# Kernel tuning notes

Measured on AMD Instinct MI355X. Metric: run time of the kernel, lower is better.

## Reference

```python
import jax, jax.numpy as jnp
import numpy as np


def _conv1x1(x, w, b=None):
    # x: [B, Cin, N, S], w: [Cout, Cin], 1x1 Conv2d
    y = jnp.einsum('oc,bcns->bons', w, x)
    if b is not None:
        y = y + b[None, :, None, None]
    return y


def setup_inputs() -> dict:
    key = jax.random.key(0)
    ks = jax.random.split(key, 16)
    B, Cin, N, K = 4, 128, 16384, 16
    MID, OUT, SHARE, PT = 64, 128, 8, 10
    s = 0.05
    inp = {
        'sm_feats': jax.random.normal(ks[0], (B, Cin, N, K), jnp.float32),
        'sm_ppfs': jax.random.normal(ks[1], (B, PT, N, K), jnp.float32),
        'conv0_w': jax.random.normal(ks[2], (OUT, Cin), jnp.float32) * s,
        'conv0_b': jax.random.normal(ks[3], (OUT,), jnp.float32) * s,
        'conv1_w': jax.random.normal(ks[4], (MID, OUT), jnp.float32) * s,
        'conv1_b': jax.random.normal(ks[5], (MID,), jnp.float32) * s,
        'conv2_w': jax.random.normal(ks[6], (MID, OUT), jnp.float32) * s,
        'conv2_b': jax.random.normal(ks[7], (MID,), jnp.float32) * s,
        'conv3_w': jax.random.normal(ks[8], (MID, OUT), jnp.float32) * s,
        'conv3_b': jax.random.normal(ks[9], (MID,), jnp.float32) * s,
        'convw1_w': jax.random.normal(ks[10], (MID // SHARE, MID * K), jnp.float32) * s,
        'convw2_w': jax.random.normal(ks[11], (K * MID // SHARE, MID // SHARE), jnp.float32) * s,
        'convw2_b': jax.random.normal(ks[12], (K * MID // SHARE,), jnp.float32) * s,
        'convout_w': jax.random.normal(ks[13], (OUT, MID), jnp.float32) * s,
        'convout_b': jax.random.normal(ks[14], (OUT,), jnp.float32) * s,
        'pt1_w': jax.random.normal(ks[15], (MID, PT), jnp.float32) * s,
        'pt2_w': jax.random.normal(jax.random.fold_in(key, 99), (MID, MID), jnp.float32) * s,
    }
    return inp


def reference(sm_feats, sm_ppfs, conv0_w, conv0_b, conv1_w, conv1_b, conv2_w, conv2_b,
              conv3_w, conv3_b, convw1_w, convw2_w, convw2_b, convout_w, convout_b,
              pt1_w, pt2_w):
    xn = jax.nn.relu(_conv1x1(sm_feats, conv0_w, conv0_b))  # [B, OUT, N, K]
    x = xn[..., :1]                                          # center point feature
    identity = x
    x1 = _conv1x1(x, conv1_w, conv1_b)       # [B, MID, N, 1]
    x2 = _conv1x1(xn, conv2_w, conv2_b)      # [B, MID, N, K]
    x3 = _conv1x1(xn, conv3_w, conv3_b)      # [B, MID, N, K]
    ptf = _conv1x1(jax.nn.relu(_conv1x1(sm_ppfs, pt1_w)), pt2_w)  # [B, MID, N, K]
    x3 = x3 + ptf
    xfs = x1 - x2 + ptf                      # [B, MID, N, K]
    B, MID, N, K = xfs.shape
    share = MID // convw1_w.shape[0]
    xfs = jnp.transpose(xfs, (0, 1, 3, 2)).reshape(B, MID * K, 1, N)
    h = jax.nn.relu(_conv1x1(xfs, convw1_w))            # [B, MID//share, 1, N]
    w = _conv1x1(h, convw2_w, convw2_b)                  # [B, K*MID//share, 1, N]
    w = jax.nn.softmax(w.reshape(B, MID // share, K, N), axis=2)
    w = jnp.transpose(w, (0, 1, 3, 2))                   # [B, MID//share, N, K]
    w = jnp.tile(w, (1, share, 1, 1))                    # [B, MID, N, K]
    out = jax.nn.relu(jnp.sum(w * x3, axis=3, keepdims=True))  # [B, MID, N, 1]
    out = (_conv1x1(out, convout_w, convout_b) + identity).squeeze(3)  # [B, OUT, N]
    return out
```

## Files before the change

kernel.cpp:

```cpp
#include <hip/hip_runtime.h>
#include <hip/hip_bf16.h>


typedef __attribute__((ext_vector_type(8))) short bf16x8;
typedef __attribute__((ext_vector_type(4))) float f32x4;
typedef __attribute__((ext_vector_type(4))) unsigned short us4;

#define MFMA(a, b, c) __builtin_amdgcn_mfma_f32_16x16x32_bf16((a), (b), (c), 0, 0, 0)

#define OFF_F    0
#define OFF_X2   0
#define OFF_PTF  17408
#define OFF_XN   34816
#define OFF_X3   34816
#define OFF_XFS  52224
#define OFF_P    69632
#define OFF_WS   69632
#define OFF_HB   74752
#define OFF_OM   76288
#define OFF_X1   77824
#define OFF_XC   78912
#define SMEM_BYTES 81088

#define WS_W0  0
#define WS_W1  16384
#define WS_W2  24576
#define WS_W3  32768
#define WS_P1  40960
#define WS_P2  43008
#define WS_CW1 47104
#define WS_WO  63488
#define WS_TOTAL 71680

__device__ __forceinline__ unsigned short f2b(float f) {
    union { __hip_bfloat16 h; unsigned short u; } v;
    v.h = __float2bfloat16(f);
    return v.u;
}
__device__ __forceinline__ float b2f(unsigned short u) {
    union { unsigned u; float f; } v;
    v.u = ((unsigned)u) << 16;
    return v.f;
}
__device__ __forceinline__ us4 pk4(float a, float b, float c, float d) {
    us4 r; r[0] = f2b(a); r[1] = f2b(b); r[2] = f2b(c); r[3] = f2b(d); return r;
}
__device__ __forceinline__ bf16x8 ldb(const unsigned short* p) {
    return *(const bf16x8*)p;
}

__global__ __launch_bounds__(512, 1)
void convert_weights(const float* __restrict__ w0, const float* __restrict__ w1,
                     const float* __restrict__ w2, const float* __restrict__ w3,
                     const float* __restrict__ p1, const float* __restrict__ p2,
                     const float* __restrict__ cw1, const float* __restrict__ wo,
                     unsigned short* __restrict__ ws) {
    int i = blockIdx.x * 512 + threadIdx.x;
    if (i >= WS_TOTAL) return;
    float v;
    if (i < 16384)      v = w0[i];
    else if (i < 24576) v = w1[i - 16384];
    else if (i < 32768) v = w2[i - 24576];
    else if (i < 40960) v = w3[i - 32768];
    else if (i < 43008) { int r = i - 40960, row = r >> 5, k = r & 31;
                          v = (k < 10) ? p1[row * 10 + k] : 0.f; }
    else if (i < 47104) v = p2[i - 43008];
    else if (i < 63488) { int r = i - 47104, j = r >> 10, kc = r & 1023;
                          v = (j < 8) ? cw1[j * 1024 + (kc & 63) * 16 + (kc >> 6)] : 0.f; }
    else                v = wo[i - 63488];
    ws[i] = f2b(v);
}

__global__ __launch_bounds__(512, 4)
void fused_model_kernel(const float* __restrict__ feats, const float* __restrict__ ppfs,
                        const unsigned short* __restrict__ wsb,
                        const float* __restrict__ b0, const float* __restrict__ b1,
                        const float* __restrict__ b2, const float* __restrict__ b3,
                        const float* __restrict__ cw2, const float* __restrict__ cb2,
                        const float* __restrict__ bo, float* __restrict__ out) {
    extern __shared__ char smem[];
    const int tid = threadIdx.x;
    const int W = tid >> 6;
    const int lane = tid & 63;
    const int kk = lane & 15;
    const int g = lane >> 4;
    const int bid = blockIdx.x;
    const int b = bid >> 11;
    const int n0 = (bid & 2047) * 8;

    bf16x8 a0[4], rA[4], rB[4];
    {
        const int mtr = (W & 3);
        #pragma unroll
        for (int kt = 0; kt < 4; ++kt) {
            a0[kt] = ldb(wsb + WS_W0 + (16 * W + kk) * 128 + kt * 32 + 8 * g);
            if (W < 4) {
                rA[kt] = ldb(wsb + WS_W3 + (16 * mtr + kk) * 128 + kt * 32 + 8 * g);
                rB[kt] = ldb(wsb + WS_W1 + (16 * mtr + kk) * 128 + kt * 32 + 8 * g);
            } else {
                rA[kt] = ldb(wsb + WS_W2 + (16 * mtr + kk) * 128 + kt * 32 + 8 * g);
                rB[kt] = ldb(wsb + WS_W3 + (16 * mtr + kk) * 128 + kt * 32 + 8 * g);
            }
        }
    }

    {
        const int kq = tid & 3, ci = tid >> 2;
        const int cisw = (ci * 2) ^ (kq << 4);
        #pragma unroll
        for (int pos = 0; pos < 8; ++pos) {
            f32x4 v = *(const f32x4*)(feats + (((size_t)b * 128 + ci) * 16384 + (n0 + pos)) * 16 + kq * 4);
            char* base = smem + OFF_F + pos * 4352 + cisw;
            *(unsigned short*)(base + (kq * 4 + 0) * 272) = f2b(v[0]);
            *(unsigned short*)(base + (kq * 4 + 1) * 272) = f2b(v[1]);
            *(unsigned short*)(base + (kq * 4 + 2) * 272) = f2b(v[2]);
            *(unsigned short*)(base + (kq * 4 + 3) * 272) = f2b(v[3]);
        }
        if (tid < 320) {
            int pos = tid / 40, r = tid % 40, p = r >> 2, kq2 = r & 3;
            f32x4 v = *(const f32x4*)(ppfs + (((size_t)b * 10 + p) * 16384 + (n0 + pos)) * 16 + kq2 * 4);
            char* base = smem + OFF_P + pos * 1024 + p * 2;
            *(unsigned short*)(base + (kq2 * 4 + 0) * 64) = f2b(v[0]);
            *(unsigned short*)(base + (kq2 * 4 + 1) * 64) = f2b(v[1]);
            *(unsigned short*)(base + (kq2 * 4 + 2) * 64) = f2b(v[2]);
            *(unsigned short*)(base + (kq2 * 4 + 3) * 64) = f2b(v[3]);
        } else {
            for (int z = tid - 320; z < 1408; z += 192) {
                int pos = z / 176, rr = z % 176, ks = rr / 11, dw = rr % 11;
                *(unsigned*)(smem + OFF_P + pos * 1024 + ks * 64 + 20 + dw * 4) = 0u;
            }
        }
    }
    __syncthreads();

    {
        f32x4 bv = *(const f32x4*)(b0 + 16 * W + 4 * g);
        const int fsw = ((kk >> 2) & 3) << 4;
        __builtin_amdgcn_s_setprio(1);
        #pragma unroll
        for (int pos = 0; pos < 8; ++pos) {
            f32x4 acc = {0.f, 0.f, 0.f, 0.f};
            #pragma unroll
            for (int kt = 0; kt < 4; ++kt) {
                bf16x8 bf = *(const bf16x8*)(smem + OFF_F + pos * 4352 + kk * 272 + ((kt * 64 + 16 * g) ^ fsw));
                acc = MFMA(a0[kt], bf, acc);
            }
            us4 xw = pk4(fmaxf(acc[0] + bv[0], 0.f), fmaxf(acc[1] + bv[1], 0.f),
                         fmaxf(acc[2] + bv[2], 0.f), fmaxf(acc[3] + bv[3], 0.f));
            *(us4*)(smem + OFF_XN + pos * 4352 + kk * 272 + (16 * W + 4 * g) * 2) = xw;
            if (kk == 0) *(us4*)(smem + OFF_XC + pos * 272 + (16 * W + 4 * g) * 2) = xw;
        }
        __builtin_amdgcn_s_setprio(0);
    }
    bf16x8 a1f[4], a2f0[4], a2f1[4];
    if (W < 4) {
        #pragma unroll
        for (int mt = 0; mt < 4; ++mt) {
            a1f[mt]  = ldb(wsb + WS_P1 + (16 * mt + kk) * 32 + 8 * g);
            a2f0[mt] = ldb(wsb + WS_P2 + (16 * mt + kk) * 64 + 8 * g);
            a2f1[mt] = ldb(wsb + WS_P2 + (16 * mt + kk) * 64 + 32 + 8 * g);
        }
    }
    __syncthreads();

    f32x4 acc3[4];
    if (W < 4) {
        const int sel = g >> 1;
        const int sa = kk + 16 * ((2 * g) & 3);
        const int sb = kk + 16 * ((2 * g + 1) & 3);
        __builtin_amdgcn_s_setprio(1);
        #pragma unroll
        for (int pp2 = 0; pp2 < 2; ++pp2) {
            const int pos = 2 * W + pp2;
            bf16x8 bp = *(const bf16x8*)(smem + OFF_P + pos * 1024 + kk * 64 + 16 * g);
            int pkd[4][2];
            #pragma unroll
            for (int mt = 0; mt < 4; ++mt) {
                f32x4 hv = {0.f, 0.f, 0.f, 0.f};
                hv = MFMA(a1f[mt], bp, hv);
                us4 t = pk4(fmaxf(hv[0], 0.f), fmaxf(hv[1], 0.f),
                            fmaxf(hv[2], 0.f), fmaxf(hv[3], 0.f));
                pkd[mt][0] = ((int*)&t)[0];
                pkd[mt][1] = ((int*)&t)[1];
            }
            union { int d[4]; bf16x8 v; } bh0, bh1;
            bh0.d[0] = sel ? __shfl(pkd[1][0], sa, 64) : __shfl(pkd[0][0], sa, 64);
            bh0.d[1] = sel ? __shfl(pkd[1][1], sa, 64) : __shfl(pkd[0][1], sa, 64);
            bh0.d[2] = sel ? __shfl(pkd[1][0], sb, 64) : __shfl(pkd[0][0], sb, 64);
            bh0.d[3] = sel ? __shfl(pkd[1][1], sb, 64) : __shfl(pkd[0][1], sb, 64);
            bh1.d[0] = sel ? __shfl(pkd[3][0], sa, 64) : __shfl(pkd[2][0], sa, 64);
            bh1.d[1] = sel ? __shfl(pkd[3][1], sa, 64) : __shfl(pkd[2][1], sa, 64);
            bh1.d[2] = sel ? __shfl(pkd[3][0], sb, 64) : __shfl(pkd[2][0], sb, 64);
            bh1.d[3] = sel ? __shfl(pkd[3][1], sb, 64) : __shfl(pkd[2][1], sb, 64);
            #pragma unroll
            for (int mt = 0; mt < 4; ++mt) {
                f32x4 acc = {0.f, 0.f, 0.f, 0.f};
                acc = MFMA(a2f0[mt], bh0.v, acc);
                acc = MFMA(a2f1[mt], bh1.v, acc);
                *(us4*)(smem + OFF_PTF + pos * 2176 + kk * 136 + (16 * mt + 4 * g) * 2) =
                    pk4(acc[0], acc[1], acc[2], acc[3]);
            }
        }
        #pragma unroll
        for (int pp2 = 0; pp2 < 4; ++pp2) {
            f32x4 acc = {0.f, 0.f, 0.f, 0.f};
            #pragma unroll
            for (int kt = 0; kt < 4; ++kt) {
                bf16x8 bf = *(const bf16x8*)(smem + OFF_XN + pp2 * 4352 + kk * 272 + (kt * 64 + 16 * g));
                acc = MFMA(rA[kt], bf, acc);
            }
            acc3[pp2] = acc;
        }
        f32x4 a1c = {0.f, 0.f, 0.f, 0.f};
        #pragma unroll
        for (int kt = 0; kt < 4; ++kt) {
            bf16x8 bf = *(const bf16x8*)(smem + OFF_XC + (kk & 7) * 272 + (kt * 64 + 16 * g));
            a1c = MFMA(rB[kt], bf, a1c);
        }
        __builtin_amdgcn_s_setprio(0);
        if (kk < 8) {
            f32x4 b1v = *(const f32x4*)(b1 + 16 * W + 4 * g);
            *(us4*)(smem + OFF_X1 + kk * 136 + (16 * W + 4 * g) * 2) =
                pk4(a1c[0] + b1v[0], a1c[1] + b1v[1], a1c[2] + b1v[2], a1c[3] + b1v[3]);
        }
    } else {
        const int mt = W - 4;
        f32x4 b2v = *(const f32x4*)(b2 + 16 * mt + 4 * g);
        __builtin_amdgcn_s_setprio(1);
        #pragma unroll
        for (int pos = 0; pos < 8; ++pos) {
            bf16x8 bx[4];
            #pragma unroll
            for (int kt = 0; kt < 4; ++kt)
                bx[kt] = *(const bf16x8*)(smem + OFF_XN + pos * 4352 + kk * 272 + (kt * 64 + 16 * g));
            f32x4 acc = {0.f, 0.f, 0.f, 0.f};
            #pragma unroll
            for (int kt = 0; kt < 4; ++kt) acc = MFMA(rA[kt], bx[kt], acc);
            *(us4*)(smem + OFF_X2 + pos * 2176 + kk * 136 + (16 * mt + 4 * g) * 2) =
                pk4(acc[0] + b2v[0], acc[1] + b2v[1], acc[2] + b2v[2], acc[3] + b2v[3]);
            if (pos >= 4) {
                f32x4 c = {0.f, 0.f, 0.f, 0.f};
                #pragma unroll
                for (int kt = 0; kt < 4; ++kt) c = MFMA(rB[kt], bx[kt], c);
                acc3[pos - 4] = c;
            }
        }
        __builtin_amdgcn_s_setprio(0);
    }
    __syncthreads();

    {
        const int mt = W & 3, ph = W >> 2;
        f32x4 b3v = *(const f32x4*)(b3 + 16 * mt + 4 * g);
        const int rot = (32 * mt + 8 * g + 16 * kk) & 127;
        #pragma unroll
        for (int pp2 = 0; pp2 < 4; ++pp2) {
            const int pos = ph * 4 + pp2;
            us4 ptfv = *(const us4*)(smem + OFF_PTF + pos * 2176 + kk * 136 + (16 * mt + 4 * g) * 2);
            us4 x2v  = *(const us4*)(smem + OFF_X2  + pos * 2176 + kk * 136 + (16 * mt + 4 * g) * 2);
            us4 x1v  = *(const us4*)(smem + OFF_X1  + pos * 136 + (16 * mt + 4 * g) * 2);
            float pf0 = b2f(ptfv[0]), pf1 = b2f(ptfv[1]), pf2 = b2f(ptfv[2]), pf3 = b2f(ptfv[3]);
            *(us4*)(smem + OFF_X3 + pos * 2176 + kk * 136 + (16 * mt + 4 * g) * 2) =
                pk4(acc3[pp2][0] + b3v[0] + pf0, acc3[pp2][1] + b3v[1] + pf1,
                    acc3[pp2][2] + b3v[2] + pf2, acc3[pp2][3] + b3v[3] + pf3);
            *(us4*)(smem + OFF_XFS + pos * 2080 + kk * 128 + rot) =
                pk4(b2f(x1v[0]) - b2f(x2v[0]) + pf0, b2f(x1v[1]) - b2f(x2v[1]) + pf1,
                    b2f(x1v[2]) - b2f(x2v[2]) + pf2, b2f(x1v[3]) - b2f(x2v[3]) + pf3);
        }
        if (tid < 64) *(float*)(smem + OFF_HB + tid * 4) = 0.f;
    }
    bf16x8 acw[4];
    {
        #pragma unroll
        for (int kt = 0; kt < 4; ++kt)
            acw[kt] = ldb(wsb + WS_CW1 + kk * 1024 + W * 128 + kt * 32 + 8 * g);
    }
    __syncthreads();

    {
        const char* xb = smem + OFF_XFS + (kk & 7) * 2080;
        f32x4 acc = {0.f, 0.f, 0.f, 0.f};
        #pragma unroll
        for (int kt = 0; kt < 4; ++kt) {
            const int k = 2 * W + (kt >> 1);
            const int byt = (64 * (kt & 1) + 16 * g + 16 * k) & 127;
            bf16x8 bf = *(const bf16x8*)(xb + k * 128 + byt);
            acc = MFMA(acw[kt], bf, acc);
        }
        if (kk < 8 && g < 2) {
            #pragma unroll
            for (int r = 0; r < 4; ++r)
                atomicAdd((float*)(smem + OFF_HB + kk * 32 + (4 * g + r) * 4), acc[r]);
        }
    }
    __syncthreads();

    bf16x8 woF[2];
    woF[0] = ldb(wsb + WS_WO + (16 * W + kk) * 64 + 8 * g);
    woF[1] = ldb(wsb + WS_WO + (16 * W + kk) * 64 + 32 + 8 * g);
    {
        const int pos = W;
        f32x4 h0 = *(const f32x4*)(smem + OFF_HB + pos * 32);
        f32x4 h1 = *(const f32x4*)(smem + OFF_HB + pos * 32 + 16);
        #pragma unroll
        for (int r = 0; r < 4; ++r) { h0[r] = fmaxf(h0[r], 0.f); h1[r] = fmaxf(h1[r], 0.f); }
        #pragma unroll
        for (int it = 0; it < 2; ++it) {
            const int c = it * 64 + lane;
            float wl = cb2[c];
            f32x4 w20 = *(const f32x4*)(cw2 + c * 8);
            f32x4 w21 = *(const f32x4*)(cw2 + c * 8 + 4);
            #pragma unroll
            for (int j = 0; j < 4; ++j) {
                wl += w20[j] * h0[j];
                wl += w21[j] * h1[j];
            }
            float mx = wl;
            for (int off = 8; off; off >>= 1) mx = fmaxf(mx, __shfl_xor(mx, off, 16));
            float e = __expf(wl - mx);
            float ss = e;
            for (int off = 8; off; off >>= 1) ss += __shfl_xor(ss, off, 16);
            *(float*)(smem + OFF_WS + pos * 640 + (4 * it + g) * 80 + kk * 4) = e / ss;
        }
        __builtin_amdgcn_wave_barrier();
        __builtin_amdgcn_sched_barrier(0);

        const char* wsp = smem + OFF_WS + pos * 640 + (lane & 7) * 80;
        f32x4 wv0 = *(const f32x4*)(wsp);
        f32x4 wv1 = *(const f32x4*)(wsp + 16);
        f32x4 wv2 = *(const f32x4*)(wsp + 32);
        f32x4 wv3 = *(const f32x4*)(wsp + 48);
        const char* x3b = smem + OFF_X3 + pos * 2176 + lane * 2;
        float s = 0.f;
        #pragma unroll
        for (int k = 0; k < 4; ++k) s += wv0[k] * b2f(*(const unsigned short*)(x3b + k * 136));
        #pragma unroll
        for (int k = 0; k < 4; ++k) s += wv1[k] * b2f(*(const unsigned short*)(x3b + (k + 4) * 136));
        #pragma unroll
        for (int k = 0; k < 4; ++k) s += wv2[k] * b2f(*(const unsigned short*)(x3b + (k + 8) * 136));
        #pragma unroll
        for (int k = 0; k < 4; ++k) s += wv3[k] * b2f(*(const unsigned short*)(x3b + (k + 12) * 136));
        *(unsigned short*)(smem + OFF_OM + pos * 144 + lane * 2) = f2b(fmaxf(s, 0.f));
    }
    __syncthreads();

    {
        f32x4 acc = {0.f, 0.f, 0.f, 0.f};
        #pragma unroll
        for (int kt = 0; kt < 2; ++kt) {
            bf16x8 bf = *(const bf16x8*)(smem + OFF_OM + (kk & 7) * 144 + (kt * 64 + 16 * g));
            acc = MFMA(woF[kt], bf, acc);
        }
        if (kk < 8) {
            f32x4 bv = *(const f32x4*)(bo + 16 * W + 4 * g);
            us4 xcv = *(const us4*)(smem + OFF_XC + kk * 272 + (16 * W + 4 * g) * 2);
            #pragma unroll
            for (int r = 0; r < 4; ++r) {
                int o = 16 * W + 4 * g + r;
                out[((size_t)b * 128 + o) * 16384 + n0 + kk] = acc[r] + bv[r] + b2f(xcv[r]);
            }
        }
    }
}

extern "C" void kernel_launch(void* const* d_in, const int* in_sizes, int n_in,
                              void* d_out, int out_size, void* d_ws, size_t ws_size,
                              hipStream_t stream) {
    (void)in_sizes; (void)n_in; (void)out_size; (void)ws_size;
    const float* feats = (const float*)d_in[0];
    const float* ppfs  = (const float*)d_in[1];
    const float* w0  = (const float*)d_in[2];
    const float* b0  = (const float*)d_in[3];
    const float* w1  = (const float*)d_in[4];
    const float* b1  = (const float*)d_in[5];
    const float* w2  = (const float*)d_in[6];
    const float* b2  = (const float*)d_in[7];
    const float* w3  = (const float*)d_in[8];
    const float* b3  = (const float*)d_in[9];
    const float* cw1 = (const float*)d_in[10];
    const float* cw2 = (const float*)d_in[11];
    const float* cb2 = (const float*)d_in[12];
    const float* wo  = (const float*)d_in[13];
    const float* bo  = (const float*)d_in[14];
    const float* p1  = (const float*)d_in[15];
    const float* p2  = (const float*)d_in[16];
    float* out = (float*)d_out;
    unsigned short* wsb = (unsigned short*)d_ws;

    convert_weights<<<dim3((WS_TOTAL + 511) / 512), dim3(512), 0, stream>>>(
        w0, w1, w2, w3, p1, p2, cw1, wo, wsb);

    (void)hipFuncSetAttribute(reinterpret_cast<const void*>(fused_model_kernel),
                              hipFuncAttributeMaxDynamicSharedMemorySize, SMEM_BYTES);
    fused_model_kernel<<<dim3(8192), dim3(512), SMEM_BYTES, stream>>>(
        feats, ppfs, wsb, b0, b1, b2, b3, cw2, cb2, bo, out);
}
```

Baseline: 301.3 us.

## Process four tiles per block and prefetch next tile's inputs during compute

Each block now loops over four 8-point tiles instead of one, cutting the grid from 8192 to 2048 blocks. The per-block weight fragments stay in registers across tiles. The next tile's feats and ppfs are loaded into shared memory during the final stages of the current tile. Shared-memory regions are rearranged so the prefetch target (OFF_F/OFF_P) does not overlap buffers still live in later stages. The intent is to amortise weight loads and block launch overhead and to overlap global loads with compute, at the cost of fewer blocks for load balancing and loads that are not truly asynchronous.

Result: slower. 662.8 us (+120.0%).

```diff
diff --git a/kernel.cpp b/kernel.cpp
--- a/kernel.cpp
+++ b/kernel.cpp
@@ -14,13 +14,13 @@
 #define OFF_XN   34816
 #define OFF_X3   34816
 #define OFF_XFS  52224
+#define OFF_WS   52224
+#define OFF_OM   57344
 #define OFF_P    69632
-#define OFF_WS   69632
-#define OFF_HB   74752
-#define OFF_OM   76288
 #define OFF_X1   77824
 #define OFF_XC   78912
-#define SMEM_BYTES 81088
+#define OFF_HB   81088
+#define SMEM_BYTES 81344
 
 #define WS_W0  0
 #define WS_W1  16384
@@ -85,8 +85,11 @@
     const int kk = lane & 15;
     const int g = lane >> 4;
     const int bid = blockIdx.x;
-    const int b = bid >> 11;
-    const int n0 = (bid & 2047) * 8;
+    const int b = bid >> 9;
+    const int n0base = (bid & 511) * 32;
+
+    const int kq = tid & 3, ci = tid >> 2;
+    const int cisw = (ci * 2) ^ (kq << 4);
 
     bf16x8 a0[4], rA[4], rB[4];
     {
@@ -103,13 +106,10 @@
             }
         }
     }
-
     {
-        const int kq = tid & 3, ci = tid >> 2;
-        const int cisw = (ci * 2) ^ (kq << 4);
         #pragma unroll
         for (int pos = 0; pos < 8; ++pos) {
-            f32x4 v = *(const f32x4*)(feats + (((size_t)b * 128 + ci) * 16384 + (n0 + pos)) * 16 + kq * 4);
+            f32x4 v = *(const f32x4*)(feats + (((size_t)b * 128 + ci) * 16384 + (n0base + pos)) * 16 + kq * 4);
             char* base = smem + OFF_F + pos * 4352 + cisw;
             *(unsigned short*)(base + (kq * 4 + 0) * 272) = f2b(v[0]);
             *(unsigned short*)(base + (kq * 4 + 1) * 272) = f2b(v[1]);
@@ -118,7 +118,7 @@
         }
         if (tid < 320) {
             int pos = tid / 40, r = tid % 40, p = r >> 2, kq2 = r & 3;
-            f32x4 v = *(const f32x4*)(ppfs + (((size_t)b * 10 + p) * 16384 + (n0 + pos)) * 16 + kq2 * 4);
+            f32x4 v = *(const f32x4*)(ppfs + (((size_t)b * 10 + p) * 16384 + (n0base + pos)) * 16 + kq2 * 4);
             char* base = smem + OFF_P + pos * 1024 + p * 2;
             *(unsigned short*)(base + (kq2 * 4 + 0) * 64) = f2b(v[0]);
             *(unsigned short*)(base + (kq2 * 4 + 1) * 64) = f2b(v[1]);
@@ -133,233 +133,260 @@
     }
     __syncthreads();
 
-    {
-        f32x4 bv = *(const f32x4*)(b0 + 16 * W + 4 * g);
-        const int fsw = ((kk >> 2) & 3) << 4;
-        __builtin_amdgcn_s_setprio(1);
-        #pragma unroll
-        for (int pos = 0; pos < 8; ++pos) {
+    #pragma unroll 1
+    for (int tt = 0; tt < 4; ++tt) {
+        const int n0 = n0base + tt * 8;
+
+        {
+            f32x4 bv = *(const f32x4*)(b0 + 16 * W + 4 * g);
+            const int fsw = ((kk >> 2) & 3) << 4;
+            __builtin_amdgcn_s_setprio(1);
+            #pragma unroll
+            for (int pos = 0; pos < 8; ++pos) {
+                f32x4 acc = {0.f, 0.f, 0.f, 0.f};
+                #pragma unroll
+                for (int kt = 0; kt < 4; ++kt) {
+                    bf16x8 bf = *(const bf16x8*)(smem + OFF_F + pos * 4352 + kk * 272 + ((kt * 64 + 16 * g) ^ fsw));
+                    acc = MFMA(a0[kt], bf, acc);
+                }
+                us4 xw = pk4(fmaxf(acc[0] + bv[0], 0.f), fmaxf(acc[1] + bv[1], 0.f),
+                             fmaxf(acc[2] + bv[2], 0.f), fmaxf(acc[3] + bv[3], 0.f));
+                *(us4*)(smem + OFF_XN + pos * 4352 + kk * 272 + (16 * W + 4 * g) * 2) = xw;
+                if (kk == 0) *(us4*)(smem + OFF_XC + pos * 272 + (16 * W + 4 * g) * 2) = xw;
+            }
+            __builtin_amdgcn_s_setprio(0);
+        }
+        bf16x8 a1f[4], a2f0[4], a2f1[4];
+        if (W < 4) {
+            #pragma unroll
+            for (int mt = 0; mt < 4; ++mt) {
+                a1f[mt]  = ldb(wsb + WS_P1 + (16 * mt + kk) * 32 + 8 * g);
+                a2f0[mt] = ldb(wsb + WS_P2 + (16 * mt + kk) * 64 + 8 * g);
+                a2f1[mt] = ldb(wsb + WS_P2 + (16 * mt + kk) * 64 + 32 + 8 * g);
+            }
+        }
+        __syncthreads();
+
+        f32x4 acc3[4];
+        if (W < 4) {
+            const int sel = g >> 1;
+            const int sa = kk + 16 * ((2 * g) & 3);
+            const int sb = kk + 16 * ((2 * g + 1) & 3);
+            __builtin_amdgcn_s_setprio(1);
+            #pragma unroll
+            for (int pp2 = 0; pp2 < 2; ++pp2) {
+                const int pos = 2 * W + pp2;
+                bf16x8 bp = *(const bf16x8*)(smem + OFF_P + pos * 1024 + kk * 64 + 16 * g);
+                int pkd[4][2];
+                #pragma unroll
+                for (int mt = 0; mt < 4; ++mt) {
+                    f32x4 hv = {0.f, 0.f, 0.f, 0.f};
+                    hv = MFMA(a1f[mt], bp, hv);
+                    us4 t = pk4(fmaxf(hv[0], 0.f), fmaxf(hv[1], 0.f),
+                                fmaxf(hv[2], 0.f), fmaxf(hv[3], 0.f));
+                    pkd[mt][0] = ((int*)&t)[0];
+                    pkd[mt][1] = ((int*)&t)[1];
+                }
+                union { int d[4]; bf16x8 v; } bh0, bh1;
+                bh0.d[0] = sel ? __shfl(pkd[1][0], sa, 64) : __shfl(pkd[0][0], sa, 64);
+                bh0.d[1] = sel ? __shfl(pkd[1][1], sa, 64) : __shfl(pkd[0][1], sa, 64);
+                bh0.d[2] = sel ? __shfl(pkd[1][0], sb, 64) : __shfl(pkd[0][0], sb, 64);
+                bh0.d[3] = sel ? __shfl(pkd[1][1], sb, 64) : __shfl(pkd[0][1], sb, 64);
+                bh1.d[0] = sel ? __shfl(pkd[3][0], sa, 64) : __shfl(pkd[2][0], sa, 64);
+                bh1.d[1] = sel ? __shfl(pkd[3][1], sa, 64) : __shfl(pkd[2][1], sa, 64);
+                bh1.d[2] = sel ? __shfl(pkd[3][0], sb, 64) : __shfl(pkd[2][0], sb, 64);
+                bh1.d[3] = sel ? __shfl(pkd[3][1], sb, 64) : __shfl(pkd[2][1], sb, 64);
+                #pragma unroll
+                for (int mt = 0; mt < 4; ++mt) {
+                    f32x4 acc = {0.f, 0.f, 0.f, 0.f};
+                    acc = MFMA(a2f0[mt], bh0.v, acc);
+                    acc = MFMA(a2f1[mt], bh1.v, acc);
+                    *(us4*)(smem + OFF_PTF + pos * 2176 + kk * 136 + (16 * mt + 4 * g) * 2) =
+                        pk4(acc[0], acc[1], acc[2], acc[3]);
+                }
+            }
+            #pragma unroll
+            for (int pp2 = 0; pp2 < 4; ++pp2) {
+                f32x4 acc = {0.f, 0.f, 0.f, 0.f};
+                #pragma unroll
+                for (int kt = 0; kt < 4; ++kt) {
+                    bf16x8 bf = *(const bf16x8*)(smem + OFF_XN + pp2 * 4352 + kk * 272 + (kt * 64 + 16 * g));
+                    acc = MFMA(rA[kt], bf, acc);
+                }
+                acc3[pp2] = acc;
+            }
+            f32x4 a1c = {0.f, 0.f, 0.f, 0.f};
+            #pragma unroll
+            for (int kt = 0; kt < 4; ++kt) {
+                bf16x8 bf = *(const bf16x8*)(smem + OFF_XC + (kk & 7) * 272 + (kt * 64 + 16 * g));
+                a1c = MFMA(rB[kt], bf, a1c);
+            }
+            __builtin_amdgcn_s_setprio(0);
+            if (kk < 8) {
+                f32x4 b1v = *(const f32x4*)(b1 + 16 * W + 4 * g);
+                *(us4*)(smem + OFF_X1 + kk * 136 + (16 * W + 4 * g) * 2) =
+                    pk4(a1c[0] + b1v[0], a1c[1] + b1v[1], a1c[2] + b1v[2], a1c[3] + b1v[3]);
+            }
+        } else {
+            const int mt = W - 4;
+            f32x4 b2v = *(const f32x4*)(b2 + 16 * mt + 4 * g);
+            __builtin_amdgcn_s_setprio(1);
+            #pragma unroll
+            for (int pos = 0; pos < 8; ++pos) {
+                bf16x8 bx[4];
+                #pragma unroll
+                for (int kt = 0; kt < 4; ++kt)
+                    bx[kt] = *(const bf16x8*)(smem + OFF_XN + pos * 4352 + kk * 272 + (kt * 64 + 16 * g));
+                f32x4 acc = {0.f, 0.f, 0.f, 0.f};
+                #pragma unroll
+                for (int kt = 0; kt < 4; ++kt) acc = MFMA(rA[kt], bx[kt], acc);
+                *(us4*)(smem + OFF_X2 + pos * 2176 + kk * 136 + (16 * mt + 4 * g) * 2) =
+                    pk4(acc[0] + b2v[0], acc[1] + b2v[1], acc[2] + b2v[2], acc[3] + b2v[3]);
+                if (pos >= 4) {
+                    f32x4 c = {0.f, 0.f, 0.f, 0.f};
+                    #pragma unroll
+                    for (int kt = 0; kt < 4; ++kt) c = MFMA(rB[kt], bx[kt], c);
+                    acc3[pos - 4] = c;
+                }
+            }
+            __builtin_amdgcn_s_setprio(0);
+        }
+        __syncthreads();
+
+        {
+            const int mt = W & 3, ph = W >> 2;
+            f32x4 b3v = *(const f32x4*)(b3 + 16 * mt + 4 * g);
+            const int rot = (32 * mt + 8 * g + 16 * kk) & 127;
+            #pragma unroll
+            for (int pp2 = 0; pp2 < 4; ++pp2) {
+                const int pos = ph * 4 + pp2;
+                us4 ptfv = *(const us4*)(smem + OFF_PTF + pos * 2176 + kk * 136 + (16 * mt + 4 * g) * 2);
+                us4 x2v  = *(const us4*)(smem + OFF_X2  + pos * 2176 + kk * 136 + (16 * mt + 4 * g) * 2);
+                us4 x1v  = *(const us4*)(smem + OFF_X1  + pos * 136 + (16 * mt + 4 * g) * 2);
+                float pf0 = b2f(ptfv[0]), pf1 = b2f(ptfv[1]), pf2 = b2f(ptfv[2]), pf3 = b2f(ptfv[3]);
+                *(us4*)(smem + OFF_X3 + pos * 2176 + kk * 136 + (16 * mt + 4 * g) * 2) =
+                    pk4(acc3[pp2][0] + b3v[0] + pf0, acc3[pp2][1] + b3v[1] + pf1,
+                        acc3[pp2][2] + b3v[2] + pf2, acc3[pp2][3] + b3v[3] + pf3);
+                *(us4*)(smem + OFF_XFS + pos * 2080 + kk * 128 + rot) =
+                    pk4(b2f(x1v[0]) - b2f(x2v[0]) + pf0, b2f(x1v[1]) - b2f(x2v[1]) + pf1,
+                        b2f(x1v[2]) - b2f(x2v[2]) + pf2, b2f(x1v[3]) - b2f(x2v[3]) + pf3);
+            }
+            if (tid < 64) *(float*)(smem + OFF_HB + tid * 4) = 0.f;
+        }
+        bf16x8 acw[4];
+        {
+            #pragma unroll
+            for (int kt = 0; kt < 4; ++kt)
+                acw[kt] = ldb(wsb + WS_CW1 + kk * 1024 + W * 128 + kt * 32 + 8 * g);
+        }
+        __syncthreads();
+
+        {
+            const char* xb = smem + OFF_XFS + (kk & 7) * 2080;
             f32x4 acc = {0.f, 0.f, 0.f, 0.f};
             #pragma unroll
             for (int kt = 0; kt < 4; ++kt) {
-                bf16x8 bf = *(const bf16x8*)(smem + OFF_F + pos * 4352 + kk * 272 + ((kt * 64 + 16 * g) ^ fsw));
-                acc = MFMA(a0[kt], bf, acc);
-            }
-            us4 xw = pk4(fmaxf(acc[0] + bv[0], 0.f), fmaxf(acc[1] + bv[1], 0.f),
-                         fmaxf(acc[2] + bv[2], 0.f), fmaxf(acc[3] + bv[3], 0.f));
-            *(us4*)(smem + OFF_XN + pos * 4352 + kk * 272 + (16 * W + 4 * g) * 2) = xw;
-            if (kk == 0) *(us4*)(smem + OFF_XC + pos * 272 + (16 * W + 4 * g) * 2) = xw;
-        }
-        __builtin_amdgcn_s_setprio(0);
-    }
-    bf16x8 a1f[4], a2f0[4], a2f1[4];
-    if (W < 4) {
-        #pragma unroll
-        for (int mt = 0; mt < 4; ++mt) {
-            a1f[mt]  = ldb(wsb + WS_P1 + (16 * mt + kk) * 32 + 8 * g);
-            a2f0[mt] = ldb(wsb + WS_P2 + (16 * mt + kk) * 64 + 8 * g);
-            a2f1[mt] = ldb(wsb + WS_P2 + (16 * mt + kk) * 64 + 32 + 8 * g);
-        }
-    }
-    __syncthreads();
-
-    f32x4 acc3[4];
-    if (W < 4) {
-        const int sel = g >> 1;
-        const int sa = kk + 16 * ((2 * g) & 3);
-        const int sb = kk + 16 * ((2 * g + 1) & 3);
-        __builtin_amdgcn_s_setprio(1);
-        #pragma unroll
-        for (int pp2 = 0; pp2 < 2; ++pp2) {
-            const int pos = 2 * W + pp2;
-            bf16x8 bp = *(const bf16x8*)(smem + OFF_P + pos * 1024 + kk * 64 + 16 * g);
-            int pkd[4][2];
-            #pragma unroll
-            for (int mt = 0; mt < 4; ++mt) {
-                f32x4 hv = {0.f, 0.f, 0.f, 0.f};
-                hv = MFMA(a1f[mt], bp, hv);
-                us4 t = pk4(fmaxf(hv[0], 0.f), fmaxf(hv[1], 0.f),
-                            fmaxf(hv[2], 0.f), fmaxf(hv[3], 0.f));
-                pkd[mt][0] = ((int*)&t)[0];
-                pkd[mt][1] = ((int*)&t)[1];
-            }
-            union { int d[4]; bf16x8 v; } bh0, bh1;
-            bh0.d[0] = sel ? __shfl(pkd[1][0], sa, 64) : __shfl(pkd[0][0], sa, 64);
-            bh0.d[1] = sel ? __shfl(pkd[1][1], sa, 64) : __shfl(pkd[0][1], sa, 64);
-            bh0.d[2] = sel ? __shfl(pkd[1][0], sb, 64) : __shfl(pkd[0][0], sb, 64);
-            bh0.d[3] = sel ? __shfl(pkd[1][1], sb, 64) : __shfl(pkd[0][1], sb, 64);
-            bh1.d[0] = sel ? __shfl(pkd[3][0], sa, 64) : __shfl(pkd[2][0], sa, 64);
-            bh1.d[1] = sel ? __shfl(pkd[3][1], sa, 64) : __shfl(pkd[2][1], sa, 64);
-            bh1.d[2] = sel ? __shfl(pkd[3][0], sb, 64) : __shfl(pkd[2][0], sb, 64);
-            bh1.d[3] = sel ? __shfl(pkd[3][1], sb, 64) : __shfl(pkd[2][1], sb, 64);
-            #pragma unroll
-            for (int mt = 0; mt < 4; ++mt) {
-                f32x4 acc = {0.f, 0.f, 0.f, 0.f};
-                acc = MFMA(a2f0[mt], bh0.v, acc);
-                acc = MFMA(a2f1[mt], bh1.v, acc);
-                *(us4*)(smem + OFF_PTF + pos * 2176 + kk * 136 + (16 * mt + 4 * g) * 2) =
-                    pk4(acc[0], acc[1], acc[2], acc[3]);
-            }
-        }
-        #pragma unroll
-        for (int pp2 = 0; pp2 < 4; ++pp2) {
+                const int k = 2 * W + (kt >> 1);
+                const int byt = (64 * (kt & 1) + 16 * g + 16 * k) & 127;
+                bf16x8 bf = *(const bf16x8*)(xb + k * 128 + byt);
+                acc = MFMA(acw[kt], bf, acc);
+            }
+            if (kk < 8 && g < 2) {
+                #pragma unroll
+                for (int r = 0; r < 4; ++r)
+                    atomicAdd((float*)(smem + OFF_HB + kk * 32 + (4 * g + r) * 4), acc[r]);
+            }
+            if (tt < 3) {
+                const int n1 = n0 + 8;
+                #pragma unroll
+                for (int pos = 0; pos < 8; ++pos) {
+                    f32x4 v = *(const f32x4*)(feats + (((size_t)b * 128 + ci) * 16384 + (n1 + pos)) * 16 + kq * 4);
+                    char* base = smem + OFF_F + pos * 4352 + cisw;
+                    *(unsigned short*)(base + (kq * 4 + 0) * 272) = f2b(v[0]);
+                    *(unsigned short*)(base + (kq * 4 + 1) * 272) = f2b(v[1]);
+                    *(unsigned short*)(base + (kq * 4 + 2) * 272) = f2b(v[2]);
+                    *(unsigned short*)(base + (kq * 4 + 3) * 272) = f2b(v[3]);
+                }
+                if (tid < 320) {
+                    int pos = tid / 40, r = tid % 40, p = r >> 2, kq2 = r & 3;
+                    f32x4 v = *(const f32x4*)(ppfs + (((size_t)b * 10 + p) * 16384 + (n1 + pos)) * 16 + kq2 * 4);
+                    char* base = smem + OFF_P + pos * 1024 + p * 2;
+                    *(unsigned short*)(base + (kq2 * 4 + 0) * 64) = f2b(v[0]);
+                    *(unsigned short*)(base + (kq2 * 4 + 1) * 64) = f2b(v[1]);
+                    *(unsigned short*)(base + (kq2 * 4 + 2) * 64) = f2b(v[2]);
+                    *(unsigned short*)(base + (kq2 * 4 + 3) * 64) = f2b(v[3]);
+                }
+            }
+        }
+        __syncthreads();
+
+        bf16x8 woF[2];
+        woF[0] = ldb(wsb + WS_WO + (16 * W + kk) * 64 + 8 * g);
+        woF[1] = ldb(wsb + WS_WO + (16 * W + kk) * 64 + 32 + 8 * g);
+        {
+            const int pos = W;
+            f32x4 h0 = *(const f32x4*)(smem + OFF_HB + pos * 32);
+            f32x4 h1 = *(const f32x4*)(smem + OFF_HB + pos * 32 + 16);
+            #pragma unroll
+            for (int r = 0; r < 4; ++r) { h0[r] = fmaxf(h0[r], 0.f); h1[r] = fmaxf(h1[r], 0.f); }
+            #pragma unroll
+            for (int it = 0; it < 2; ++it) {
+                const int c = it * 64 + lane;
+                float wl = cb2[c];
+                f32x4 w20 = *(const f32x4*)(cw2 + c * 8);
+                f32x4 w21 = *(const f32x4*)(cw2 + c * 8 + 4);
+                #pragma unroll
+                for (int j = 0; j < 4; ++j) {
+                    wl += w20[j] * h0[j];
+                    wl += w21[j] * h1[j];
+                }
+                float mx = wl;
+                for (int off = 8; off; off >>= 1) mx = fmaxf(mx, __shfl_xor(mx, off, 16));
+                float e = __expf(wl - mx);
+                float ss = e;
+                for (int off = 8; off; off >>= 1) ss += __shfl_xor(ss, off, 16);
+                *(float*)(smem + OFF_WS + pos * 640 + (4 * it + g) * 80 + kk * 4) = e / ss;
+            }
+            __builtin_amdgcn_wave_barrier();
+            __builtin_amdgcn_sched_barrier(0);
+
+            const char* wsp = smem + OFF_WS + pos * 640 + (lane & 7) * 80;
+            f32x4 wv0 = *(const f32x4*)(wsp);
+            f32x4 wv1 = *(const f32x4*)(wsp + 16);
+            f32x4 wv2 = *(const f32x4*)(wsp + 32);
+            f32x4 wv3 = *(const f32x4*)(wsp + 48);
+            const char* x3b = smem + OFF_X3 + pos * 2176 + lane * 2;
+            float s = 0.f;
+            #pragma unroll
+            for (int k = 0; k < 4; ++k) s += wv0[k] * b2f(*(const unsigned short*)(x3b + k * 136));
+            #pragma unroll
+            for (int k = 0; k < 4; ++k) s += wv1[k] * b2f(*(const unsigned short*)(x3b + (k + 4) * 136));
+            #pragma unroll
+            for (int k = 0; k < 4; ++k) s += wv2[k] * b2f(*(const unsigned short*)(x3b + (k + 8) * 136));
+            #pragma unroll
+            for (int k = 0; k < 4; ++k) s += wv3[k] * b2f(*(const unsigned short*)(x3b + (k + 12) * 136));
+            *(unsigned short*)(smem + OFF_OM + pos * 144 + lane * 2) = f2b(fmaxf(s, 0.f));
+        }
+        __syncthreads();
+
+        {
             f32x4 acc = {0.f, 0.f, 0.f, 0.f};
             #pragma unroll
-            for (int kt = 0; kt < 4; ++kt) {
-                bf16x8 bf = *(const bf16x8*)(smem + OFF_XN + pp2 * 4352 + kk * 272 + (kt * 64 + 16 * g));
-                acc = MFMA(rA[kt], bf, acc);
-            }
-            acc3[pp2] = acc;
-        }
-        f32x4 a1c = {0.f, 0.f, 0.f, 0.f};
-        #pragma unroll
-        for (int kt = 0; kt < 4; ++kt) {
-            bf16x8 bf = *(const bf16x8*)(smem + OFF_XC + (kk & 7) * 272 + (kt * 64 + 16 * g));
-            a1c = MFMA(rB[kt], bf, a1c);
-        }
-        __builtin_amdgcn_s_setprio(0);
-        if (kk < 8) {
-            f32x4 b1v = *(const f32x4*)(b1 + 16 * W + 4 * g);
-            *(us4*)(smem + OFF_X1 + kk * 136 + (16 * W + 4 * g) * 2) =
-                pk4(a1c[0] + b1v[0], a1c[1] + b1v[1], a1c[2] + b1v[2], a1c[3] + b1v[3]);
-        }
-    } else {
-        const int mt = W - 4;
-        f32x4 b2v = *(const f32x4*)(b2 + 16 * mt + 4 * g);
-        __builtin_amdgcn_s_setprio(1);
-        #pragma unroll
-        for (int pos = 0; pos < 8; ++pos) {
-            bf16x8 bx[4];
-            #pragma unroll
-            for (int kt = 0; kt < 4; ++kt)
-                bx[kt] = *(const bf16x8*)(smem + OFF_XN + pos * 4352 + kk * 272 + (kt * 64 + 16 * g));
-            f32x4 acc = {0.f, 0.f, 0.f, 0.f};
-            #pragma unroll
-            for (int kt = 0; kt < 4; ++kt) acc = MFMA(rA[kt], bx[kt], acc);
-            *(us4*)(smem + OFF_X2 + pos * 2176 + kk * 136 + (16 * mt + 4 * g) * 2) =
-                pk4(acc[0] + b2v[0], acc[1] + b2v[1], acc[2] + b2v[2], acc[3] + b2v[3]);
-            if (pos >= 4) {
-                f32x4 c = {0.f, 0.f, 0.f, 0.f};
-                #pragma unroll
-                for (int kt = 0; kt < 4; ++kt) c = MFMA(rB[kt], bx[kt], c);
-                acc3[pos - 4] = c;
-            }
-        }
-        __builtin_amdgcn_s_setprio(0);
-    }
-    __syncthreads();
-
-    {
-        const int mt = W & 3, ph = W >> 2;
-        f32x4 b3v = *(const f32x4*)(b3 + 16 * mt + 4 * g);
-        const int rot = (32 * mt + 8 * g + 16 * kk) & 127;
-        #pragma unroll
-        for (int pp2 = 0; pp2 < 4; ++pp2) {
-            const int pos = ph * 4 + pp2;
-            us4 ptfv = *(const us4*)(smem + OFF_PTF + pos * 2176 + kk * 136 + (16 * mt + 4 * g) * 2);
-            us4 x2v  = *(const us4*)(smem + OFF_X2  + pos * 2176 + kk * 136 + (16 * mt + 4 * g) * 2);
-            us4 x1v  = *(const us4*)(smem + OFF_X1  + pos * 136 + (16 * mt + 4 * g) * 2);
-            float pf0 = b2f(ptfv[0]), pf1 = b2f(ptfv[1]), pf2 = b2f(ptfv[2]), pf3 = b2f(ptfv[3]);
-            *(us4*)(smem + OFF_X3 + pos * 2176 + kk * 136 + (16 * mt + 4 * g) * 2) =
-                pk4(acc3[pp2][0] + b3v[0] + pf0, acc3[pp2][1] + b3v[1] + pf1,
-                    acc3[pp2][2] + b3v[2] + pf2, acc3[pp2][3] + b3v[3] + pf3);
-            *(us4*)(smem + OFF_XFS + pos * 2080 + kk * 128 + rot) =
-                pk4(b2f(x1v[0]) - b2f(x2v[0]) + pf0, b2f(x1v[1]) - b2f(x2v[1]) + pf1,
-                    b2f(x1v[2]) - b2f(x2v[2]) + pf2, b2f(x1v[3]) - b2f(x2v[3]) + pf3);
-        }
-        if (tid < 64) *(float*)(smem + OFF_HB + tid * 4) = 0.f;
-    }
-    bf16x8 acw[4];
-    {
-        #pragma unroll
-        for (int kt = 0; kt < 4; ++kt)
-            acw[kt] = ldb(wsb + WS_CW1 + kk * 1024 + W * 128 + kt * 32 + 8 * g);
-    }
-    __syncthreads();
-
-    {
-        const char* xb = smem + OFF_XFS + (kk & 7) * 2080;
-        f32x4 acc = {0.f, 0.f, 0.f, 0.f};
-        #pragma unroll
-        for (int kt = 0; kt < 4; ++kt) {
-            const int k = 2 * W + (kt >> 1);
-            const int byt = (64 * (kt & 1) + 16 * g + 16 * k) & 127;
-            bf16x8 bf = *(const bf16x8*)(xb + k * 128 + byt);
-            acc = MFMA(acw[kt], bf, acc);
-        }
-        if (kk < 8 && g < 2) {
-            #pragma unroll
-            for (int r = 0; r < 4; ++r)
-                atomicAdd((float*)(smem + OFF_HB + kk * 32 + (4 * g + r) * 4), acc[r]);
-        }
-    }
-    __syncthreads();
-
-    bf16x8 woF[2];
-    woF[0] = ldb(wsb + WS_WO + (16 * W + kk) * 64 + 8 * g);
-    woF[1] = ldb(wsb + WS_WO + (16 * W + kk) * 64 + 32 + 8 * g);
-    {
-        const int pos = W;
-        f32x4 h0 = *(const f32x4*)(smem + OFF_HB + pos * 32);
-        f32x4 h1 = *(const f32x4*)(smem + OFF_HB + pos * 32 + 16);
-        #pragma unroll
-        for (int r = 0; r < 4; ++r) { h0[r] = fmaxf(h0[r], 0.f); h1[r] = fmaxf(h1[r], 0.f); }
-        #pragma unroll
-        for (int it = 0; it < 2; ++it) {
-            const int c = it * 64 + lane;
-            float wl = cb2[c];
-            f32x4 w20 = *(const f32x4*)(cw2 + c * 8);
-            f32x4 w21 = *(const f32x4*)(cw2 + c * 8 + 4);
-            #pragma unroll
-            for (int j = 0; j < 4; ++j) {
-                wl += w20[j] * h0[j];
-                wl += w21[j] * h1[j];
-            }
-            float mx = wl;
-            for (int off = 8; off; off >>= 1) mx = fmaxf(mx, __shfl_xor(mx, off, 16));
-            float e = __expf(wl - mx);
-            float ss = e;
-            for (int off = 8; off; off >>= 1) ss += __shfl_xor(ss, off, 16);
-            *(float*)(smem + OFF_WS + pos * 640 + (4 * it + g) * 80 + kk * 4) = e / ss;
-        }
-        __builtin_amdgcn_wave_barrier();
-        __builtin_amdgcn_sched_barrier(0);
-
-        const char* wsp = smem + OFF_WS + pos * 640 + (lane & 7) * 80;
-        f32x4 wv0 = *(const f32x4*)(wsp);
-        f32x4 wv1 = *(const f32x4*)(wsp + 16);
-        f32x4 wv2 = *(const f32x4*)(wsp + 32);
-        f32x4 wv3 = *(const f32x4*)(wsp + 48);
-        const char* x3b = smem + OFF_X3 + pos * 2176 + lane * 2;
-        float s = 0.f;
-        #pragma unroll
-        for (int k = 0; k < 4; ++k) s += wv0[k] * b2f(*(const unsigned short*)(x3b + k * 136));
-        #pragma unroll
-        for (int k = 0; k < 4; ++k) s += wv1[k] * b2f(*(const unsigned short*)(x3b + (k + 4) * 136));
-        #pragma unroll
-        for (int k = 0; k < 4; ++k) s += wv2[k] * b2f(*(const unsigned short*)(x3b + (k + 8) * 136));
-        #pragma unroll
-        for (int k = 0; k < 4; ++k) s += wv3[k] * b2f(*(const unsigned short*)(x3b + (k + 12) * 136));
-        *(unsigned short*)(smem + OFF_OM + pos * 144 + lane * 2) = f2b(fmaxf(s, 0.f));
-    }
-    __syncthreads();
-
-    {
-        f32x4 acc = {0.f, 0.f, 0.f, 0.f};
-        #pragma unroll
-        for (int kt = 0; kt < 2; ++kt) {
-            bf16x8 bf = *(const bf16x8*)(smem + OFF_OM + (kk & 7) * 144 + (kt * 64 + 16 * g));
-            acc = MFMA(woF[kt], bf, acc);
-        }
-        if (kk < 8) {
-            f32x4 bv = *(const f32x4*)(bo + 16 * W + 4 * g);
-            us4 xcv = *(const us4*)(smem + OFF_XC + kk * 272 + (16 * W + 4 * g) * 2);
-            #pragma unroll
-            for (int r = 0; r < 4; ++r) {
-                int o = 16 * W + 4 * g + r;
-                out[((size_t)b * 128 + o) * 16384 + n0 + kk] = acc[r] + bv[r] + b2f(xcv[r]);
-            }
-        }
+            for (int kt = 0; kt < 2; ++kt) {
+                bf16x8 bf = *(const bf16x8*)(smem + OFF_OM + (kk & 7) * 144 + (kt * 64 + 16 * g));
+                acc = MFMA(woF[kt], bf, acc);
+            }
+            if (kk < 8) {
+                f32x4 bv = *(const f32x4*)(bo + 16 * W + 4 * g);
+                us4 xcv = *(const us4*)(smem + OFF_XC + kk * 272 + (16 * W + 4 * g) * 2);
+                #pragma unroll
+                for (int r = 0; r < 4; ++r) {
+                    int o = 16 * W + 4 * g + r;
+                    out[((size_t)b * 128 + o) * 16384 + n0 + kk] = acc[r] + bv[r] + b2f(xcv[r]);
+                }
+            }
+        }
+        if (tt != 3) __syncthreads();
     }
 }
 
@@ -392,6 +419,6 @@
 
     (void)hipFuncSetAttribute(reinterpret_cast<const void*>(fused_model_kernel),
                               hipFuncAttributeMaxDynamicSharedMemorySize, SMEM_BYTES);
-    fused_model_kernel<<<dim3(8192), dim3(512), SMEM_BYTES, stream>>>(
+    fused_model_kernel<<<dim3(2048), dim3(512), SMEM_BYTES, stream>>>(
         feats, ppfs, wsb, b0, b1, b2, b3, cw2, cb2, bo, out);
 }
```
